# Performance work log

Measured on AMD Instinct MI355X. Metric: run time of the kernel, lower is better.

Reference implementation:

```python
import jax, jax.numpy as jnp
import numpy as np

K = 3        # kernel_size
STRIDE = 1
PAD = 1
BASIS = 8    # act_fun.get_size()


def cheb_basis(x):
    """Chebyshev polynomial basis T_0..T_{BASIS-1} of tanh(x); appends basis axis."""
    t = jnp.tanh(x)
    polys = [jnp.ones_like(t), t]
    for _ in range(BASIS - 2):
        polys.append(2.0 * t * polys[-1] - polys[-2])
    return jnp.stack(polys, axis=-1)  # (..., BASIS)


def silu(x):
    return x * jax.nn.sigmoid(x)


def unfold(x):
    """torch F.unfold equivalent: (b,c,h,w) -> (b, c, K*K, L), L = ho*wo."""
    b, c, h, w = x.shape
    ho = (h - K + 2 * PAD) // STRIDE + 1
    wo = (w - K + 2 * PAD) // STRIDE + 1
    xp = jnp.pad(x, ((0, 0), (0, 0), (PAD, PAD), (PAD, PAD)))
    pats = [xp[:, :, i:i + STRIDE * ho:STRIDE, j:j + STRIDE * wo:STRIDE]
            for i in range(K) for j in range(K)]
    pats = jnp.stack(pats, axis=2)  # (b, c, K*K, ho, wo)
    return pats.reshape(b, c, K * K, ho * wo), ho, wo


def setup_inputs() -> dict:
    key = jax.random.key(0)
    k1, k2, k3 = jax.random.split(key, 3)
    cin, cout = 64, 64
    x = jax.random.normal(k1, (16, cin, 32, 32), dtype=jnp.float32)
    # xavier_normal_ on (in,out,k^2,1): std = sqrt(2/(fan_in+fan_out)) approx
    w = jax.random.normal(k2, (cin, cout, K * K), dtype=jnp.float32) * jnp.sqrt(2.0 / (cin + cout))
    # normal_(c, 0, 0.1) on (in,out,k^2,1,basis) -> squeeze the broadcast dim
    c = jax.random.normal(k3, (cin, cout, K * K, BASIS), dtype=jnp.float32) * 0.1
    return {"x": x, "w": w, "c": c}


def reference(x, w, c):
    b = x.shape[0]
    pats, ho, wo = unfold(x)          # (b, i, k, l)
    res = silu(pats)                  # residual activation path
    act = cheb_basis(pats)            # (b, i, k, l, s) spline basis
    # sum_i sum_k w[i,o,k] * res[b,i,k,l]
    term1 = jnp.einsum('iok,bikl->bol', w, res)
    # sum_i sum_k sum_s w[i,o,k]*c[i,o,k,s]*act[b,i,k,l,s] (fused, avoids (b,i,o,k,l,s))
    cw = c * w[..., None]             # (i, o, k, s)
    term2 = jnp.einsum('ioks,bikls->bol', cw, act)
    return (term1 + term2).reshape(b, -1, ho, wo)
```

## Files before the change

### kernel.cpp

```cpp
#include <hip/hip_runtime.h>
#include <hip/hip_bf16.h>


#define CIN   64
#define COUT  64
#define HW    32
#define LL    1024
#define NS    8

typedef __attribute__((ext_vector_type(8))) short short8;
typedef __attribute__((ext_vector_type(4))) float f32x4;

typedef const __attribute__((address_space(1))) void gvoid_t;
typedef __attribute__((address_space(3))) void lvoid_t;


__global__ void prep_kernel(const float* __restrict__ w,
                            const float* __restrict__ c,
                            __hip_bfloat16* __restrict__ Wt,
                            float* __restrict__ bias) {
    int bx = blockIdx.x;
    if (bx >= 144) {
        const int o = bx - 144;
        const int i = threadIdx.x;
        if (i >= 64) return;
        float v = 0.f;
#pragma unroll
        for (int k = 0; k < 9; ++k) {
            const int idx = (i * COUT + o) * 9 + k;
            v += w[idx] * c[idx * 8];
        }
#pragma unroll
        for (int off = 32; off > 0; off >>= 1) v += __shfl_down(v, off);
        if (i == 0) bias[o] = v;
        return;
    }
    const int tid = bx * 256 + threadIdx.x;
    const int i = tid / (9 * COUT);
    const int r = tid - i * 9 * COUT;
    const int k = r / COUT;
    const int o = r - k * COUT;
    const int widx = (i * COUT + o) * 9 + k;
    const float wv = w[widx];
    __hip_bfloat16* dst = Wt + (size_t)tid * NS;
    dst[0] = __float2bfloat16(wv);
#pragma unroll
    for (int s = 1; s < 8; ++s) dst[s] = __float2bfloat16(wv * c[widx * 8 + s]);
}

__global__ __launch_bounds__(256, 2) void kan_fused_kernel(
        const float* __restrict__ x,
        const __hip_bfloat16* __restrict__ Wt,
        const float* __restrict__ bias,
        float* __restrict__ out) {
    __shared__ __align__(16) unsigned short Wlds[31488];

    const int tid   = threadIdx.x;
    const int wv    = tid >> 6;
    const int lane  = tid & 63;
    const int quad  = lane >> 4;
    const int l16   = lane & 15;
    const int khalf = wv >> 1;
    const int pg    = wv & 1;

    const int b  = blockIdx.x;
    const int y0 = blockIdx.y * 2;
    const int oh = blockIdx.z;
    const int row = y0 + pg;

    const float4* wsrc = (const float4*)Wt;
    unsigned short* scratch = Wlds + 18432 + wv * 3264;

    f32x4 acc[2][2];
#pragma unroll
    for (int h = 0; h < 2; ++h)
#pragma unroll
        for (int nt = 0; nt < 2; ++nt) acc[h][nt] = (f32x4){0.f, 0.f, 0.f, 0.f};

    for (int step = 0; step < 8; ++step) {
        __syncthreads();
#pragma unroll
        for (int p = 0; p < 9; ++p) {
            const int j  = p * 256 + tid;
            const int kh = (j >= 1152);
            const int jj = j - (kh ? 1152 : 0);
            const int il = jj / 288;
            const int r2 = jj - il * 288;
            const int k  = r2 >> 5;
            const int oo = r2 & 31;
            const float4* src =
                wsrc + (size_t)(((kh * 32 + step * 4 + il) * 9 + k) << 6) + (oh << 5) + oo;
            __builtin_amdgcn_global_load_lds((gvoid_t*)src, (lvoid_t*)((float4*)Wlds + j), 16, 0, 0);
        }
        const int chbase = khalf * 32 + step * 4;
#pragma unroll
        for (int p = 0; p < 7; ++p) {
            const int cell = p * 64 + lane;
            if (cell < 408) {
                const int ch  = cell / 102;
                const int rem = cell - ch * 102;
                const int r3  = rem / 34;
                const int col = rem - r3 * 34;
                const int gy  = row - 1 + r3;
                const int gx  = col - 1;
                __align__(16) unsigned int u[4];
                if ((unsigned)gy < 32u && (unsigned)gx < 32u) {
                    const float xv = x[((size_t)(b * CIN + chbase + ch) * HW + gy) * HW + gx];
                    const float e   = __expf(-xv);
                    const float res = xv / (1.f + e);
                    const float e2  = __expf(2.f * xv);
                    const float t   = 1.f - 2.f / (e2 + 1.f);
                    const float T2 = 2.f * t * t  - 1.f;
                    const float T3 = 2.f * t * T2 - t;
                    const float T4 = 2.f * t * T3 - T2;
                    const float T5 = 2.f * t * T4 - T3;
                    const float T6 = 2.f * t * T5 - T4;
                    const float T7 = 2.f * t * T6 - T5;
                    __hip_bfloat16* hv = (__hip_bfloat16*)u;
                    hv[0] = __float2bfloat16(res); hv[1] = __float2bfloat16(t);
                    hv[2] = __float2bfloat16(T2);  hv[3] = __float2bfloat16(T3);
                    hv[4] = __float2bfloat16(T4);  hv[5] = __float2bfloat16(T5);
                    hv[6] = __float2bfloat16(T6);  hv[7] = __float2bfloat16(T7);
                } else {
                    u[0] = 0x00000000u; u[1] = 0x0000BF80u;
                    u[2] = 0x00003F80u; u[3] = 0x0000BF80u;
                }
                *(float4*)(scratch + cell * 8) = *(const float4*)u;
            }
        }
        __syncthreads();

        const unsigned short* wb = Wlds + khalf * 9216;
#pragma unroll
        for (int kpos = 0; kpos < 9; ++kpos) {
            const int dy = kpos / 3 - 1, dx = kpos % 3 - 1;
            const int cb = quad * 102 + (dy + 1) * 34 + (dx + 1);
            short8 af0 = *(const short8*)(scratch + (cb + l16) * 8);
            short8 af1 = *(const short8*)(scratch + (cb + 16 + l16) * 8);
#pragma unroll
            for (int nt = 0; nt < 2; ++nt) {
                short8 wf = *(const short8*)(wb + ((quad * 9 + kpos) * 32 + nt * 16 + l16) * NS);
                acc[0][nt] = __builtin_amdgcn_mfma_f32_16x16x32_bf16(wf, af0, acc[0][nt], 0, 0, 0);
                acc[1][nt] = __builtin_amdgcn_mfma_f32_16x16x32_bf16(wf, af1, acc[1][nt], 0, 0, 0);
            }
        }
    }

    __syncthreads();
    float* red = (float*)Wlds;
#pragma unroll
    for (int h = 0; h < 2; ++h)
#pragma unroll
        for (int nt = 0; nt < 2; ++nt)
#pragma unroll
            for (int r = 0; r < 4; ++r) {
                const int pixl = pg * 32 + h * 16 + l16;
                const int ol   = nt * 16 + quad * 4 + r;
                red[(khalf * 64 + pixl) * 33 + ol] = acc[h][nt][r];
            }
    __syncthreads();

#pragma unroll
    for (int rep2 = 0; rep2 < 8; ++rep2) {
        const int v = rep2 * 256 + tid;
        const int pixl = v & 63;
        const int ol   = v >> 6;
        const int o    = (oh << 5) + ol;
        const float s  = red[pixl * 33 + ol] + red[(64 + pixl) * 33 + ol] + bias[o];
        out[(size_t)(b * COUT + o) * LL + (y0 + (pixl >> 5)) * HW + (pixl & 31)] = s;
    }
}

extern "C" void kernel_launch(void* const* d_in, const int* in_sizes, int n_in,
                              void* d_out, int out_size, void* d_ws, size_t ws_size,
                              hipStream_t stream) {
    const float* x = (const float*)d_in[0];
    const float* w = (const float*)d_in[1];
    const float* c = (const float*)d_in[2];
    float* out = (float*)d_out;

    char* ws = (char*)d_ws;
    __hip_bfloat16* Wt   = (__hip_bfloat16*)(ws);
    float*          bias = (float*)(ws + 589824);

    prep_kernel<<<208, 256, 0, stream>>>(w, c, Wt, bias);
    kan_fused_kernel<<<dim3(16, 16, 2), 256, 0, stream>>>(x, Wt, bias, out);
}
```

Before: 89.66 us.

## Split input channels across waves, load weights directly from global, drop LDS staging

Each block now handles a single output row, and each of its four waves covers a quarter of the input channels, so no block-wide barriers are needed inside the channel loop. Weight fragments are read straight from global memory (relying on L2/L1 caching) instead of being staged into LDS with global_load_lds. The smaller LDS footprint allows four blocks per CU, and the grid doubles. The trade-off is more scattered global weight traffic and a four-way cross-wave reduction at the end.

```diff
diff --git a/kernel.cpp b/kernel.cpp
--- a/kernel.cpp
+++ b/kernel.cpp
@@ -10,9 +10,6 @@
 
 typedef __attribute__((ext_vector_type(8))) short short8;
 typedef __attribute__((ext_vector_type(4))) float f32x4;
-
-typedef const __attribute__((address_space(1))) void gvoid_t;
-typedef __attribute__((address_space(3))) void lvoid_t;
 
 
 __global__ void prep_kernel(const float* __restrict__ w,
@@ -48,28 +45,25 @@
     for (int s = 1; s < 8; ++s) dst[s] = __float2bfloat16(wv * c[widx * 8 + s]);
 }
 
-__global__ __launch_bounds__(256, 2) void kan_fused_kernel(
+__global__ __launch_bounds__(256, 4) void kan_fused_kernel(
         const float* __restrict__ x,
         const __hip_bfloat16* __restrict__ Wt,
         const float* __restrict__ bias,
         float* __restrict__ out) {
-    __shared__ __align__(16) unsigned short Wlds[31488];
+    __shared__ __align__(16) unsigned short Wlds[13056];
 
     const int tid   = threadIdx.x;
     const int wv    = tid >> 6;
     const int lane  = tid & 63;
     const int quad  = lane >> 4;
     const int l16   = lane & 15;
-    const int khalf = wv >> 1;
-    const int pg    = wv & 1;
 
-    const int b  = blockIdx.x;
-    const int y0 = blockIdx.y * 2;
-    const int oh = blockIdx.z;
-    const int row = y0 + pg;
+    const int b   = blockIdx.x;
+    const int row = blockIdx.y;
+    const int oh  = blockIdx.z;
 
-    const float4* wsrc = (const float4*)Wt;
-    unsigned short* scratch = Wlds + 18432 + wv * 3264;
+    const unsigned short* WtU = (const unsigned short*)Wt;
+    unsigned short* scratch = Wlds + wv * 3264;
 
     f32x4 acc[2][2];
 #pragma unroll
@@ -77,22 +71,8 @@
 #pragma unroll
         for (int nt = 0; nt < 2; ++nt) acc[h][nt] = (f32x4){0.f, 0.f, 0.f, 0.f};
 
-    for (int step = 0; step < 8; ++step) {
-        __syncthreads();
-#pragma unroll
-        for (int p = 0; p < 9; ++p) {
-            const int j  = p * 256 + tid;
-            const int kh = (j >= 1152);
-            const int jj = j - (kh ? 1152 : 0);
-            const int il = jj / 288;
-            const int r2 = jj - il * 288;
-            const int k  = r2 >> 5;
-            const int oo = r2 & 31;
-            const float4* src =
-                wsrc + (size_t)(((kh * 32 + step * 4 + il) * 9 + k) << 6) + (oh << 5) + oo;
-            __builtin_amdgcn_global_load_lds((gvoid_t*)src, (lvoid_t*)((float4*)Wlds + j), 16, 0, 0);
-        }
-        const int chbase = khalf * 32 + step * 4;
+    for (int chunk = 0; chunk < 4; ++chunk) {
+        const int chbase = wv * 16 + chunk * 4;
 #pragma unroll
         for (int p = 0; p < 7; ++p) {
             const int cell = p * 64 + lane;
@@ -128,9 +108,9 @@
                 *(float4*)(scratch + cell * 8) = *(const float4*)u;
             }
         }
-        __syncthreads();
 
-        const unsigned short* wb = Wlds + khalf * 9216;
+        const unsigned short* wchunk = WtU +
+            ((size_t)(chbase + quad) * 9 * COUT + (oh << 5) + l16) * NS;
 #pragma unroll
         for (int kpos = 0; kpos < 9; ++kpos) {
             const int dy = kpos / 3 - 1, dx = kpos % 3 - 1;
@@ -139,7 +119,7 @@
             short8 af1 = *(const short8*)(scratch + (cb + 16 + l16) * 8);
 #pragma unroll
             for (int nt = 0; nt < 2; ++nt) {
-                short8 wf = *(const short8*)(wb + ((quad * 9 + kpos) * 32 + nt * 16 + l16) * NS);
+                short8 wf = *(const short8*)(wchunk + (kpos * COUT + nt * 16) * NS);
                 acc[0][nt] = __builtin_amdgcn_mfma_f32_16x16x32_bf16(wf, af0, acc[0][nt], 0, 0, 0);
                 acc[1][nt] = __builtin_amdgcn_mfma_f32_16x16x32_bf16(wf, af1, acc[1][nt], 0, 0, 0);
             }
@@ -154,20 +134,21 @@
         for (int nt = 0; nt < 2; ++nt)
 #pragma unroll
             for (int r = 0; r < 4; ++r) {
-                const int pixl = pg * 32 + h * 16 + l16;
-                const int ol   = nt * 16 + quad * 4 + r;
-                red[(khalf * 64 + pixl) * 33 + ol] = acc[h][nt][r];
+                const int p  = h * 16 + l16;
+                const int ol = nt * 16 + quad * 4 + r;
+                red[(wv * 32 + p) * 33 + ol] = acc[h][nt][r];
             }
     __syncthreads();
 
 #pragma unroll
-    for (int rep2 = 0; rep2 < 8; ++rep2) {
-        const int v = rep2 * 256 + tid;
-        const int pixl = v & 63;
-        const int ol   = v >> 6;
-        const int o    = (oh << 5) + ol;
-        const float s  = red[pixl * 33 + ol] + red[(64 + pixl) * 33 + ol] + bias[o];
-        out[(size_t)(b * COUT + o) * LL + (y0 + (pixl >> 5)) * HW + (pixl & 31)] = s;
+    for (int rep = 0; rep < 4; ++rep) {
+        const int v  = rep * 256 + tid;
+        const int p  = v & 31;
+        const int ol = v >> 5;
+        const int o  = (oh << 5) + ol;
+        const float s = red[p * 33 + ol] + red[(32 + p) * 33 + ol]
+                      + red[(64 + p) * 33 + ol] + red[(96 + p) * 33 + ol] + bias[o];
+        out[(size_t)(b * COUT + o) * LL + row * HW + p] = s;
     }
 }
 
@@ -184,5 +165,5 @@
     float*          bias = (float*)(ws + 589824);
 
     prep_kernel<<<208, 256, 0, stream>>>(w, c, Wt, bias);
-    kan_fused_kernel<<<dim3(16, 16, 2), 256, 0, stream>>>(x, Wt, bias, out);
+    kan_fused_kernel<<<dim3(16, 32, 2), 256, 0, stream>>>(x, Wt, bias, out);
 }
```

After: 85.81 us. -4.3%, faster.
